# Performance work log

Hardware: AMD Instinct MI355X
Metric: run time of the kernel (lower is better)

Reference implementation:

```python
import jax, jax.numpy as jnp
import numpy as np

N_NODES = 100000
N_EDGES = 1600000
F_IN = 64
HIDDEN = 128
N_GRAPHS = 1024
EPS = 1e-5  # BatchNorm1d eps


def setup_inputs() -> dict:
    key = jax.random.key(0)
    ks = jax.random.split(key, 16)
    inp = {
        "x": jax.random.normal(ks[0], (N_NODES, F_IN), jnp.float32),
        "edge_index": jax.random.randint(ks[1], (2, N_EDGES), 0, N_NODES, dtype=jnp.int32),
        "edge_attr": jax.random.uniform(ks[2], (N_EDGES, 1), jnp.float32),
        "batch": jnp.sort(jax.random.randint(ks[3], (N_NODES,), 0, N_GRAPHS, dtype=jnp.int32)),
    }
    dims = [F_IN, HIDDEN, HIDDEN]
    for i in range(3):
        d_in = dims[i]
        kk = jax.random.split(ks[4 + i], 2)
        s = 1.0 / np.sqrt(d_in).astype(np.float32)
        inp[f"rel_w{i}"] = jax.random.uniform(kk[0], (d_in, HIDDEN), jnp.float32, -s, s)
        inp[f"rel_b{i}"] = jnp.zeros((HIDDEN,), jnp.float32)
        inp[f"root_w{i}"] = jax.random.uniform(kk[1], (d_in, HIDDEN), jnp.float32, -s, s)
        inp[f"bn_g{i}"] = jnp.ones((HIDDEN,), jnp.float32)
        inp[f"bn_b{i}"] = jnp.zeros((HIDDEN,), jnp.float32)
        inp[f"bn_m{i}"] = jnp.zeros((HIDDEN,), jnp.float32)
        inp[f"bn_v{i}"] = jnp.ones((HIDDEN,), jnp.float32)
    inp["head_w1"] = jax.random.uniform(ks[8], (HIDDEN, HIDDEN // 2), jnp.float32, -0.1, 0.1)
    inp["head_b1"] = jnp.zeros((HIDDEN // 2,), jnp.float32)
    inp["head_w2"] = jax.random.uniform(ks[9], (HIDDEN // 2, 1), jnp.float32, -0.1, 0.1)
    inp["head_b2"] = jnp.zeros((1,), jnp.float32)
    return inp


def _graph_conv(h, src, dst, ew, w_rel, b_rel, w_root):
    # PyG GraphConv (aggr='add'): lin_rel(sum_j e_ji * x_j) + lin_root(x_i)
    msg = h[src] * ew[:, None]                                   # [E, in] gather
    agg = jax.ops.segment_sum(msg, dst, num_segments=h.shape[0])  # [N, in] scatter-add
    return agg @ w_rel + b_rel + h @ w_root


def reference(x, edge_index, edge_attr, batch,
              rel_w0, rel_b0, root_w0, bn_g0, bn_b0, bn_m0, bn_v0,
              rel_w1, rel_b1, root_w1, bn_g1, bn_b1, bn_m1, bn_v1,
              rel_w2, rel_b2, root_w2, bn_g2, bn_b2, bn_m2, bn_v2,
              head_w1, head_b1, head_w2, head_b2):
    src, dst = edge_index[0], edge_index[1]
    ew = edge_attr[:, 0]
    layers = [
        (rel_w0, rel_b0, root_w0, bn_g0, bn_b0, bn_m0, bn_v0),
        (rel_w1, rel_b1, root_w1, bn_g1, bn_b1, bn_m1, bn_v1),
        (rel_w2, rel_b2, root_w2, bn_g2, bn_b2, bn_m2, bn_v2),
    ]
    h = x
    for (wr, br, wo, g, b, m, v) in layers:
        h = _graph_conv(h, src, dst, ew, wr, br, wo)
        # BatchNorm1d in eval mode (running stats) + ReLU; dropout is identity in eval
        h = jax.nn.relu((h - m) * (g * jax.lax.rsqrt(v + EPS)) + b)
    # global_mean_pool over graph assignment ids
    sums = jax.ops.segment_sum(h, batch, num_segments=N_GRAPHS)                       # [G, H]
    cnts = jax.ops.segment_sum(jnp.ones((h.shape[0],), h.dtype), batch, num_segments=N_GRAPHS)
    pooled = sums / jnp.maximum(cnts, 1.0)[:, None]
    hid = jax.nn.relu(pooled @ head_w1 + head_b1)
    out = hid @ head_w2 + head_b2
    return out[:, 0]
```

## Files before the change

kernel.cpp:

```cpp
#include <hip/hip_runtime.h>

#define N_NODES 100000
#define N_EDGES 1600000
#define F_IN 64
#define HIDDEN 128
#define N_GRAPHS 1024
#define EPS 1e-5f

typedef short short8 __attribute__((ext_vector_type(8)));
typedef float f32x4 __attribute__((ext_vector_type(4)));
typedef unsigned int uint;
typedef unsigned short ushort;

__device__ __forceinline__ ushort f2b(float f) {
    uint x = __float_as_uint(f);
    return (ushort)((x + 0x7fffu + ((x >> 16) & 1u)) >> 16);
}
__device__ __forceinline__ uint pack2(float a, float b) {
    return (uint)f2b(a) | ((uint)f2b(b) << 16);
}
__device__ __forceinline__ float b2f_lo(uint u) { return __uint_as_float(u << 16); }
__device__ __forceinline__ float b2f_hi(uint u) { return __uint_as_float(u & 0xffff0000u); }

#define NBLK_A 128
#define CHUNK ((N_EDGES + NBLK_A - 1) / NBLK_A)
#define BUCK_SHIFT 9
#define NBUCK ((N_NODES + 511) / 512)
#define SCAN_M (NBUCK * NBLK_A)


__global__ __launch_bounds__(256) void bin_count_kernel(const int* __restrict__ ei,
                                                        int* __restrict__ counts) {
    __shared__ int cnt[NBUCK];
    int blk = blockIdx.x, t = threadIdx.x;
    for (int i = t; i < NBUCK; i += 256) cnt[i] = 0;
    __syncthreads();
    int e0 = blk * CHUNK, e1 = min(e0 + CHUNK, N_EDGES);
    for (int e = e0 + t; e < e1; e += 256)
        atomicAdd(&cnt[ei[N_EDGES + e] >> BUCK_SHIFT], 1);
    __syncthreads();
    for (int i = t; i < NBUCK; i += 256) counts[i * NBLK_A + blk] = cnt[i];
}

__global__ __launch_bounds__(1024) void scan_counts_kernel(int* __restrict__ counts,
                                                           int* __restrict__ rowptr) {
    __shared__ int tot[1024];
    const int PT = (SCAN_M + 1023) / 1024;
    int t = threadIdx.x;
    int base = t * PT;
    int local[PT];
    int s = 0;
    #pragma unroll
    for (int i = 0; i < PT; ++i) {
        int idx = base + i;
        int v = (idx < SCAN_M) ? counts[idx] : 0;
        local[i] = s;
        s += v;
    }
    tot[t] = s;
    __syncthreads();
    int v = s;
    for (int off = 1; off < 1024; off <<= 1) {
        int x = (t >= off) ? tot[t - off] : 0;
        __syncthreads();
        tot[t] += x;
        __syncthreads();
    }
    int excl = tot[t] - v;
    #pragma unroll
    for (int i = 0; i < PT; ++i) {
        int idx = base + i;
        if (idx < SCAN_M) counts[idx] = excl + local[i];
    }
    if (t == 0) rowptr[N_NODES] = N_EDGES;
}

__global__ __launch_bounds__(256) void bin_scatter_kernel(const int* __restrict__ ei,
                                                          const float* __restrict__ ea,
                                                          const int* __restrict__ counts,
                                                          int* __restrict__ dstb,
                                                          int2* __restrict__ emb) {
    __shared__ int cur[NBUCK];
    int blk = blockIdx.x, t = threadIdx.x;
    for (int i = t; i < NBUCK; i += 256) cur[i] = counts[i * NBLK_A + blk];
    __syncthreads();
    int e0 = blk * CHUNK, e1 = min(e0 + CHUNK, N_EDGES);
    for (int e = e0 + t; e < e1; e += 256) {
        int s = ei[e], d = ei[N_EDGES + e];
        float w = ea[e];
        int p = atomicAdd(&cur[d >> BUCK_SHIFT], 1);
        dstb[p] = d;
        emb[p] = make_int2(s, __float_as_int(w));
    }
}

__global__ __launch_bounds__(1024) void bucket_build_kernel(const int* __restrict__ counts,
                                                            const int* __restrict__ dstb,
                                                            const int2* __restrict__ emb,
                                                            int* __restrict__ rowptr,
                                                            int2* __restrict__ em) {
    __shared__ int hist[512];
    __shared__ int cursor[512];
    int b = blockIdx.x, t = threadIdx.x;
    int beg = counts[b * NBLK_A];
    int end = (b + 1 < NBUCK) ? counts[(b + 1) * NBLK_A] : N_EDGES;
    int nbase = b << BUCK_SHIFT;
    int nnodes = min(512, N_NODES - nbase);

    if (t < 512) hist[t] = 0;
    __syncthreads();
    for (int e = beg + t; e < end; e += 1024)
        atomicAdd(&hist[dstb[e] & 511], 1);
    __syncthreads();

    int v = (t < 512) ? hist[t] : 0;
    for (int off = 1; off < 512; off <<= 1) {
        int x = (t < 512 && t >= off) ? hist[t - off] : 0;
        __syncthreads();
        if (t < 512) hist[t] += x;
        __syncthreads();
    }
    if (t < 512) {
        int excl = hist[t] - v;
        cursor[t] = beg + excl;
        if (t < nnodes) rowptr[nbase + t] = beg + excl;
    }
    __syncthreads();

    for (int e = beg + t; e < end; e += 1024) {
        int d = dstb[e];
        int2 m = emb[e];
        int p = atomicAdd(&cursor[d & 511], 1);
        em[p] = m;
    }
}


__global__ __launch_bounds__(256) void cvt_x_kernel(const float* __restrict__ x,
                                                    ushort* __restrict__ xb) {
    int i = blockIdx.x * 256 + threadIdx.x;
    if (i < N_NODES * 32) {
        float2 v = ((const float2*)x)[i];
        ((uint*)xb)[i] = pack2(v.x, v.y);
    }
}

__global__ __launch_bounds__(256) void cvt_w_kernel(const float* __restrict__ W0,
                                                    const float* __restrict__ W1,
                                                    int F, ushort* __restrict__ Wb) {
    int K = 2 * F;
    int idx = blockIdx.x * 256 + threadIdx.x;
    if (idx >= 64 * K) return;
    int c  = idx / (K / 2);
    int k2 = (idx % (K / 2)) * 2;
    float f0 = (k2 < F) ? W0[k2 * 128 + c] : W1[(k2 - F) * 128 + c];
    float f1 = (k2 + 1 < F) ? W0[(k2 + 1) * 128 + c] : W1[(k2 + 1 - F) * 128 + c];
    ((uint*)Wb)[idx] = pack2(f0, f1);
}


template <int F>
__global__ __launch_bounds__(256) void agg_kernel(const ushort* __restrict__ h,
                                                  const int* __restrict__ rowptr,
                                                  const int2* __restrict__ em,
                                                  ushort* __restrict__ agg) {
    int node = blockIdx.x * 4 + (threadIdx.x >> 6);
    int lane = threadIdx.x & 63;
    int g  = lane >> 4;
    int sl = lane & 15;
    int beg = rowptr[node], end = rowptr[node + 1];
    int e = beg;

    if (F == 128) {
        float acc[8] = {};
        for (; e + 8 <= end; e += 8) {
            int2 mA = em[e + g];
            int2 mB = em[e + 4 + g];
            uint4 vA = *(const uint4*)(h + (size_t)mA.x * 128 + sl * 8);
            uint4 vB = *(const uint4*)(h + (size_t)mB.x * 128 + sl * 8);
            float wA = __int_as_float(mA.y), wB = __int_as_float(mB.y);
            acc[0] = fmaf(b2f_lo(vA.x), wA, acc[0]);
            acc[1] = fmaf(b2f_hi(vA.x), wA, acc[1]);
            acc[2] = fmaf(b2f_lo(vA.y), wA, acc[2]);
            acc[3] = fmaf(b2f_hi(vA.y), wA, acc[3]);
            acc[4] = fmaf(b2f_lo(vA.z), wA, acc[4]);
            acc[5] = fmaf(b2f_hi(vA.z), wA, acc[5]);
            acc[6] = fmaf(b2f_lo(vA.w), wA, acc[6]);
            acc[7] = fmaf(b2f_hi(vA.w), wA, acc[7]);
            acc[0] = fmaf(b2f_lo(vB.x), wB, acc[0]);
            acc[1] = fmaf(b2f_hi(vB.x), wB, acc[1]);
            acc[2] = fmaf(b2f_lo(vB.y), wB, acc[2]);
            acc[3] = fmaf(b2f_hi(vB.y), wB, acc[3]);
            acc[4] = fmaf(b2f_lo(vB.z), wB, acc[4]);
            acc[5] = fmaf(b2f_hi(vB.z), wB, acc[5]);
            acc[6] = fmaf(b2f_lo(vB.w), wB, acc[6]);
            acc[7] = fmaf(b2f_hi(vB.w), wB, acc[7]);
        }
        for (; e < end; e += 4) {
            int ej = e + g;
            if (ej < end) {
                int2 m = em[ej];
                uint4 v = *(const uint4*)(h + (size_t)m.x * 128 + sl * 8);
                float w = __int_as_float(m.y);
                acc[0] = fmaf(b2f_lo(v.x), w, acc[0]);
                acc[1] = fmaf(b2f_hi(v.x), w, acc[1]);
                acc[2] = fmaf(b2f_lo(v.y), w, acc[2]);
                acc[3] = fmaf(b2f_hi(v.y), w, acc[3]);
                acc[4] = fmaf(b2f_lo(v.z), w, acc[4]);
                acc[5] = fmaf(b2f_hi(v.z), w, acc[5]);
                acc[6] = fmaf(b2f_lo(v.w), w, acc[6]);
                acc[7] = fmaf(b2f_hi(v.w), w, acc[7]);
            }
        }
        #pragma unroll
        for (int f = 0; f < 8; ++f) {
            acc[f] += __shfl_xor(acc[f], 16);
            acc[f] += __shfl_xor(acc[f], 32);
        }
        if (lane < 16) {
            uint4 o;
            o.x = pack2(acc[0], acc[1]);
            o.y = pack2(acc[2], acc[3]);
            o.z = pack2(acc[4], acc[5]);
            o.w = pack2(acc[6], acc[7]);
            *(uint4*)(agg + (size_t)node * 128 + sl * 8) = o;
        }
    } else {
        float acc[4] = {};
        for (; e + 8 <= end; e += 8) {
            int2 mA = em[e + g];
            int2 mB = em[e + 4 + g];
            uint2 vA = *(const uint2*)(h + (size_t)mA.x * 64 + sl * 4);
            uint2 vB = *(const uint2*)(h + (size_t)mB.x * 64 + sl * 4);
            float wA = __int_as_float(mA.y), wB = __int_as_float(mB.y);
            acc[0] = fmaf(b2f_lo(vA.x), wA, acc[0]);
            acc[1] = fmaf(b2f_hi(vA.x), wA, acc[1]);
            acc[2] = fmaf(b2f_lo(vA.y), wA, acc[2]);
            acc[3] = fmaf(b2f_hi(vA.y), wA, acc[3]);
            acc[0] = fmaf(b2f_lo(vB.x), wB, acc[0]);
            acc[1] = fmaf(b2f_hi(vB.x), wB, acc[1]);
            acc[2] = fmaf(b2f_lo(vB.y), wB, acc[2]);
            acc[3] = fmaf(b2f_hi(vB.y), wB, acc[3]);
        }
        for (; e < end; e += 4) {
            int ej = e + g;
            if (ej < end) {
                int2 m = em[ej];
                uint2 v = *(const uint2*)(h + (size_t)m.x * 64 + sl * 4);
                float w = __int_as_float(m.y);
                acc[0] = fmaf(b2f_lo(v.x), w, acc[0]);
                acc[1] = fmaf(b2f_hi(v.x), w, acc[1]);
                acc[2] = fmaf(b2f_lo(v.y), w, acc[2]);
                acc[3] = fmaf(b2f_hi(v.y), w, acc[3]);
            }
        }
        #pragma unroll
        for (int f = 0; f < 4; ++f) {
            acc[f] += __shfl_xor(acc[f], 16);
            acc[f] += __shfl_xor(acc[f], 32);
        }
        if (lane < 16) {
            uint2 o;
            o.x = pack2(acc[0], acc[1]);
            o.y = pack2(acc[2], acc[3]);
            *(uint2*)(agg + (size_t)node * 64 + sl * 4) = o;
        }
    }
}


template <int F>
__global__ __launch_bounds__(256, 2) void gemm_mfma(const ushort* __restrict__ A0,
                                                    const ushort* __restrict__ A1,
                                                    const ushort* __restrict__ Wb,
                                                    const float* __restrict__ bias,
                                                    const float* __restrict__ bng,
                                                    const float* __restrict__ bnb,
                                                    const float* __restrict__ bnm,
                                                    const float* __restrict__ bnv,
                                                    ushort* __restrict__ out) {
    constexpr int K = 2 * F;
    constexpr int LDW = K + 8;
    __shared__ ushort Wl[128 * LDW];

    int t = threadIdx.x;
    for (int idx = t; idx < 128 * (K / 8); idx += 256) {
        int c  = idx / (K / 8);
        int k8 = (idx % (K / 8)) * 8;
        *(short8*)&Wl[c * LDW + k8] = *(const short8*)&Wb[c * K + k8];
    }
    __syncthreads();

    int wave = t >> 6, lane = t & 63;
    int m = lane & 15, quad = lane >> 4;
    int r0 = blockIdx.x * 128 + wave * 32 + m;
    int r1 = r0 + 16;

    f32x4 acc0[8], acc1[8];
    #pragma unroll
    for (int i = 0; i < 8; ++i) { acc0[i] = (f32x4)(0.f); acc1[i] = (f32x4)(0.f); }

    auto loadA = [&](int row, int k0) -> short8 {
        short8 v = {};
        if (row < N_NODES)
            v = (k0 < F) ? *(const short8*)(A0 + (size_t)row * F + k0)
                         : *(const short8*)(A1 + (size_t)row * F + (k0 - F));
        return v;
    };

    short8 a0 = loadA(r0, quad * 8);
    short8 a1 = loadA(r1, quad * 8);
    for (int kc = 0; kc < K; kc += 32) {
        int k0 = kc + quad * 8;
        short8 na0 = {}, na1 = {};
        if (kc + 32 < K) {
            na0 = loadA(r0, k0 + 32);
            na1 = loadA(r1, k0 + 32);
        }
        #pragma unroll
        for (int ct = 0; ct < 8; ++ct) {
            short8 b = *(const short8*)&Wl[(ct * 16 + m) * LDW + k0];
            acc0[ct] = __builtin_amdgcn_mfma_f32_16x16x32_bf16(a0, b, acc0[ct], 0, 0, 0);
            acc1[ct] = __builtin_amdgcn_mfma_f32_16x16x32_bf16(a1, b, acc1[ct], 0, 0, 0);
        }
        a0 = na0; a1 = na1;
    }

    int rb0 = blockIdx.x * 128 + wave * 32 + quad * 4;
    #pragma unroll
    for (int ct = 0; ct < 8; ++ct) {
        int c = ct * 16 + m;
        float sc = bng[c] * rsqrtf(bnv[c] + EPS);
        float sh = bnb[c] - bnm[c] * sc;
        float bi = bias[c];
        #pragma unroll
        for (int reg = 0; reg < 4; ++reg) {
            int r = rb0 + reg;
            if (r < N_NODES) {
                float v = fmaxf(fmaf(acc0[ct][reg] + bi, sc, sh), 0.f);
                out[(size_t)r * 128 + c] = f2b(v);
            }
            int r2 = rb0 + 16 + reg;
            if (r2 < N_NODES) {
                float v = fmaxf(fmaf(acc1[ct][reg] + bi, sc, sh), 0.f);
                out[(size_t)r2 * 128 + c] = f2b(v);
            }
        }
    }
}


#define POOL_NODES 64
__global__ __launch_bounds__(256) void pool_kernel(const ushort* __restrict__ h,
                                                   const int* __restrict__ batch,
                                                   float* __restrict__ pooled) {
    __shared__ int gb[POOL_NODES];
    int b = blockIdx.x, t = threadIdx.x;
    int n0 = b * POOL_NODES;
    if (t < POOL_NODES) {
        int n = n0 + t;
        gb[t] = (n < N_NODES) ? batch[n] : -1;
    }
    __syncthreads();
    int f = t & 127;
    int half = t >> 7;
    float acc = 0.f;
    int gcur = -1;
    for (int i = half; i < POOL_NODES; i += 2) {
        int n = n0 + i;
        if (n >= N_NODES) break;
        int g = gb[i];
        if (g != gcur) {
            if (gcur >= 0) atomicAdd(&pooled[(size_t)gcur * 128 + f], acc);
            gcur = g;
            acc = 0.f;
        }
        acc += b2f_lo((uint)h[(size_t)n * 128 + f]);
    }
    if (gcur >= 0) atomicAdd(&pooled[(size_t)gcur * 128 + f], acc);
}


__global__ __launch_bounds__(64) void head_kernel(const float* __restrict__ pooled,
                                                  const int* __restrict__ batch,
                                                  const float* __restrict__ w1,
                                                  const float* __restrict__ b1,
                                                  const float* __restrict__ w2,
                                                  const float* __restrict__ b2,
                                                  float* __restrict__ out) {
    int g = blockIdx.x;
    int j = threadIdx.x;
    int lo = 0, hi = N_NODES;
    while (lo < hi) { int m = (lo + hi) >> 1; if (batch[m] <  g) lo = m + 1; else hi = m; }
    int start = lo;
    lo = 0; hi = N_NODES;
    while (lo < hi) { int m = (lo + hi) >> 1; if (batch[m] <= g) lo = m + 1; else hi = m; }
    float inv = 1.0f / fmaxf((float)(lo - start), 1.0f);

    float acc = b1[j];
    #pragma unroll 4
    for (int k = 0; k < 128; ++k)
        acc = fmaf(pooled[(size_t)g * 128 + k] * inv, w1[k * 64 + j], acc);
    float prod = fmaxf(acc, 0.f) * w2[j];
    #pragma unroll
    for (int off = 32; off > 0; off >>= 1)
        prod += __shfl_down(prod, off);
    if (j == 0) out[g] = prod + b2[0];
}


extern "C" void kernel_launch(void* const* d_in, const int* in_sizes, int n_in,
                              void* d_out, int out_size, void* d_ws, size_t ws_size,
                              hipStream_t stream) {
    const float* x     = (const float*)d_in[0];
    const int*   ei    = (const int*)d_in[1];
    const float* ea    = (const float*)d_in[2];
    const int*   batch = (const int*)d_in[3];
    const float* rel_w[3]  = {(const float*)d_in[4],  (const float*)d_in[11], (const float*)d_in[18]};
    const float* rel_b[3]  = {(const float*)d_in[5],  (const float*)d_in[12], (const float*)d_in[19]};
    const float* root_w[3] = {(const float*)d_in[6],  (const float*)d_in[13], (const float*)d_in[20]};
    const float* bn_g[3]   = {(const float*)d_in[7],  (const float*)d_in[14], (const float*)d_in[21]};
    const float* bn_b[3]   = {(const float*)d_in[8],  (const float*)d_in[15], (const float*)d_in[22]};
    const float* bn_m[3]   = {(const float*)d_in[9],  (const float*)d_in[16], (const float*)d_in[23]};
    const float* bn_v[3]   = {(const float*)d_in[10], (const float*)d_in[17], (const float*)d_in[24]};
    const float* head_w1 = (const float*)d_in[25];
    const float* head_b1 = (const float*)d_in[26];
    const float* head_w2 = (const float*)d_in[27];
    const float* head_b2 = (const float*)d_in[28];
    float* out = (float*)d_out;

    char* ws = (char*)d_ws;
    int*    rowptr = (int*)(ws + 0);
    int*    counts = (int*)(ws + 401408);
    int2*   em     = (int2*)(ws + 524288);
    ushort* xb     = (ushort*)(ws + 13631488);
    ushort* h_a    = (ushort*)(ws + 26431488);
    ushort* h_b    = (ushort*)(ws + 52031488);
    ushort* aggb   = (ushort*)(ws + 77631488);
    float*  pooled = (float*)(ws + 103231488);
    ushort* wb     = (ushort*)(ws + 103755776);
    int*    dstb = (int*)(ws + 77631488);
    int2*   emb  = (int2*)(ws + 84031488);

    ushort* wb0 = wb;
    ushort* wb1 = wb + 16384;
    ushort* wb2 = wb + 49152;

    hipMemsetAsync(pooled, 0, N_GRAPHS * HIDDEN * sizeof(float), stream);

    bin_count_kernel<<<NBLK_A, 256, 0, stream>>>(ei, counts);
    scan_counts_kernel<<<1, 1024, 0, stream>>>(counts, rowptr);
    bin_scatter_kernel<<<NBLK_A, 256, 0, stream>>>(ei, ea, counts, dstb, emb);
    bucket_build_kernel<<<NBUCK, 1024, 0, stream>>>(counts, dstb, emb, rowptr, em);
    cvt_x_kernel<<<(N_NODES * 32 + 255) / 256, 256, 0, stream>>>(x, xb);
    cvt_w_kernel<<<(64 * 128 + 255) / 256, 256, 0, stream>>>(rel_w[0], root_w[0], 64,  wb0);
    cvt_w_kernel<<<(64 * 256 + 255) / 256, 256, 0, stream>>>(rel_w[1], root_w[1], 128, wb1);
    cvt_w_kernel<<<(64 * 256 + 255) / 256, 256, 0, stream>>>(rel_w[2], root_w[2], 128, wb2);

    const int AGG_BLOCKS  = N_NODES / 4;
    const int GEMM_BLOCKS = (N_NODES + 127) / 128;

    agg_kernel<64><<<AGG_BLOCKS, 256, 0, stream>>>(xb, rowptr, em, aggb);
    gemm_mfma<64><<<GEMM_BLOCKS, 256, 0, stream>>>(aggb, xb, wb0, rel_b[0],
                                                   bn_g[0], bn_b[0], bn_m[0], bn_v[0], h_a);
    agg_kernel<128><<<AGG_BLOCKS, 256, 0, stream>>>(h_a, rowptr, em, aggb);
    gemm_mfma<128><<<GEMM_BLOCKS, 256, 0, stream>>>(aggb, h_a, wb1, rel_b[1],
                                                    bn_g[1], bn_b[1], bn_m[1], bn_v[1], h_b);
    agg_kernel<128><<<AGG_BLOCKS, 256, 0, stream>>>(h_b, rowptr, em, aggb);
    gemm_mfma<128><<<GEMM_BLOCKS, 256, 0, stream>>>(aggb, h_b, wb2, rel_b[2],
                                                    bn_g[2], bn_b[2], bn_m[2], bn_v[2], h_a);

    pool_kernel<<<(N_NODES + POOL_NODES - 1) / POOL_NODES, 256, 0, stream>>>(h_a, batch, pooled);
    head_kernel<<<N_GRAPHS, 64, 0, stream>>>(pooled, batch, head_w1, head_b1, head_w2, head_b2, out);
}
```

Before: 527.6 us.

## Fuse prep kernels, split scan across blocks, pack edge data, widen pool loads

Merges the x/weight bf16 conversions and the pooled zeroing into one prep kernel, which removes several launches and a memset. The single-block count scan becomes a three-kernel reduce/scan/apply across multiple blocks. Edge binning now packs a bf16 weight and the low destination bits into one word, dropping the separate dstb array and its traffic, at the cost of rounding edge weights to bf16 earlier. The pool kernel reads two features per thread with 32-bit loads.

```diff
diff --git a/kernel.cpp b/kernel.cpp
--- a/kernel.cpp
+++ b/kernel.cpp
@@ -27,6 +27,7 @@
 #define BUCK_SHIFT 9
 #define NBUCK ((N_NODES + 511) / 512)
 #define SCAN_M (NBUCK * NBLK_A)
+#define SCAN_T ((SCAN_M + 1023) / 1024)
 
 
 __global__ __launch_bounds__(256) void bin_count_kernel(const int* __restrict__ ei,
@@ -42,43 +43,53 @@
     for (int i = t; i < NBUCK; i += 256) counts[i * NBLK_A + blk] = cnt[i];
 }
 
-__global__ __launch_bounds__(1024) void scan_counts_kernel(int* __restrict__ counts,
-                                                           int* __restrict__ rowptr) {
-    __shared__ int tot[1024];
-    const int PT = (SCAN_M + 1023) / 1024;
-    int t = threadIdx.x;
-    int base = t * PT;
-    int local[PT];
-    int s = 0;
+__global__ __launch_bounds__(1024) void sc_reduce_kernel(const int* __restrict__ counts,
+                                                         int* __restrict__ partial) {
+    __shared__ int lds[16];
+    int b = blockIdx.x, t = threadIdx.x;
+    int i = b * 1024 + t;
+    int v = (i < SCAN_M) ? counts[i] : 0;
     #pragma unroll
-    for (int i = 0; i < PT; ++i) {
-        int idx = base + i;
-        int v = (idx < SCAN_M) ? counts[idx] : 0;
-        local[i] = s;
-        s += v;
-    }
-    tot[t] = s;
-    __syncthreads();
-    int v = s;
+    for (int off = 32; off > 0; off >>= 1) v += __shfl_down(v, off);
+    if ((t & 63) == 0) lds[t >> 6] = v;
+    __syncthreads();
+    if (t == 0) {
+        int s = 0;
+        #pragma unroll
+        for (int j = 0; j < 16; ++j) s += lds[j];
+        partial[b] = s;
+    }
+}
+
+__global__ __launch_bounds__(64) void sc_small_kernel(int* __restrict__ partial,
+                                                      int* __restrict__ rowptr) {
+    if (threadIdx.x == 0) {
+        int s = 0;
+        for (int j = 0; j < SCAN_T; ++j) { int v = partial[j]; partial[j] = s; s += v; }
+        rowptr[N_NODES] = N_EDGES;
+    }
+}
+
+__global__ __launch_bounds__(1024) void sc_apply_kernel(int* __restrict__ counts,
+                                                        const int* __restrict__ partial) {
+    __shared__ int lds[1024];
+    int b = blockIdx.x, t = threadIdx.x;
+    int i = b * 1024 + t;
+    int v = (i < SCAN_M) ? counts[i] : 0;
+    lds[t] = v;
+    __syncthreads();
     for (int off = 1; off < 1024; off <<= 1) {
-        int x = (t >= off) ? tot[t - off] : 0;
+        int x = (t >= off) ? lds[t - off] : 0;
         __syncthreads();
-        tot[t] += x;
+        lds[t] += x;
         __syncthreads();
     }
-    int excl = tot[t] - v;
-    #pragma unroll
-    for (int i = 0; i < PT; ++i) {
-        int idx = base + i;
-        if (idx < SCAN_M) counts[idx] = excl + local[i];
-    }
-    if (t == 0) rowptr[N_NODES] = N_EDGES;
+    if (i < SCAN_M) counts[i] = lds[t] - v + partial[b];
 }
 
 __global__ __launch_bounds__(256) void bin_scatter_kernel(const int* __restrict__ ei,
                                                           const float* __restrict__ ea,
                                                           const int* __restrict__ counts,
-                                                          int* __restrict__ dstb,
                                                           int2* __restrict__ emb) {
     __shared__ int cur[NBUCK];
     int blk = blockIdx.x, t = threadIdx.x;
@@ -87,15 +98,13 @@
     int e0 = blk * CHUNK, e1 = min(e0 + CHUNK, N_EDGES);
     for (int e = e0 + t; e < e1; e += 256) {
         int s = ei[e], d = ei[N_EDGES + e];
-        float w = ea[e];
+        uint y = ((uint)f2b(ea[e]) << 16) | (uint)(d & 511);
         int p = atomicAdd(&cur[d >> BUCK_SHIFT], 1);
-        dstb[p] = d;
-        emb[p] = make_int2(s, __float_as_int(w));
+        emb[p] = make_int2(s, (int)y);
     }
 }
 
 __global__ __launch_bounds__(1024) void bucket_build_kernel(const int* __restrict__ counts,
-                                                            const int* __restrict__ dstb,
                                                             const int2* __restrict__ emb,
                                                             int* __restrict__ rowptr,
                                                             int2* __restrict__ em) {
@@ -110,7 +119,7 @@
     if (t < 512) hist[t] = 0;
     __syncthreads();
     for (int e = beg + t; e < end; e += 1024)
-        atomicAdd(&hist[dstb[e] & 511], 1);
+        atomicAdd(&hist[(uint)emb[e].y & 511u], 1);
     __syncthreads();
 
     int v = (t < 512) ? hist[t] : 0;
@@ -128,34 +137,50 @@
     __syncthreads();
 
     for (int e = beg + t; e < end; e += 1024) {
-        int d = dstb[e];
         int2 m = emb[e];
-        int p = atomicAdd(&cursor[d & 511], 1);
-        em[p] = m;
-    }
-}
-
-
-__global__ __launch_bounds__(256) void cvt_x_kernel(const float* __restrict__ x,
-                                                    ushort* __restrict__ xb) {
-    int i = blockIdx.x * 256 + threadIdx.x;
-    if (i < N_NODES * 32) {
-        float2 v = ((const float2*)x)[i];
-        ((uint*)xb)[i] = pack2(v.x, v.y);
-    }
-}
-
-__global__ __launch_bounds__(256) void cvt_w_kernel(const float* __restrict__ W0,
-                                                    const float* __restrict__ W1,
-                                                    int F, ushort* __restrict__ Wb) {
+        int p = atomicAdd(&cursor[(uint)m.y & 511u], 1);
+        em[p] = make_int2(m.x, (int)((uint)m.y & 0xffff0000u));
+    }
+}
+
+
+#define PREP_X   (N_NODES * 32)
+#define PREP_W0  8192
+#define PREP_W1  16384
+#define PREP_W2  16384
+#define PREP_PZ  (N_GRAPHS * HIDDEN)
+#define PREP_TOT (PREP_X + PREP_W0 + PREP_W1 + PREP_W2 + PREP_PZ)
+
+__device__ __forceinline__ void cvt_w_elem(const float* W0, const float* W1, int F,
+                                           int idx, uint* out) {
     int K = 2 * F;
-    int idx = blockIdx.x * 256 + threadIdx.x;
-    if (idx >= 64 * K) return;
     int c  = idx / (K / 2);
     int k2 = (idx % (K / 2)) * 2;
     float f0 = (k2 < F) ? W0[k2 * 128 + c] : W1[(k2 - F) * 128 + c];
     float f1 = (k2 + 1 < F) ? W0[(k2 + 1) * 128 + c] : W1[(k2 + 1 - F) * 128 + c];
-    ((uint*)Wb)[idx] = pack2(f0, f1);
+    out[idx] = pack2(f0, f1);
+}
+
+__global__ __launch_bounds__(256) void prep_kernel(const float* __restrict__ x, uint* __restrict__ xb,
+                                                   const float* __restrict__ rw0, const float* __restrict__ ow0,
+                                                   const float* __restrict__ rw1, const float* __restrict__ ow1,
+                                                   const float* __restrict__ rw2, const float* __restrict__ ow2,
+                                                   uint* __restrict__ wb0, uint* __restrict__ wb1,
+                                                   uint* __restrict__ wb2, float* __restrict__ pooled) {
+    int i = blockIdx.x * 256 + threadIdx.x;
+    if (i < PREP_X) {
+        float2 v = ((const float2*)x)[i];
+        xb[i] = pack2(v.x, v.y);
+        return;
+    }
+    i -= PREP_X;
+    if (i < PREP_W0) { cvt_w_elem(rw0, ow0, 64, i, wb0); return; }
+    i -= PREP_W0;
+    if (i < PREP_W1) { cvt_w_elem(rw1, ow1, 128, i, wb1); return; }
+    i -= PREP_W1;
+    if (i < PREP_W2) { cvt_w_elem(rw2, ow2, 128, i, wb2); return; }
+    i -= PREP_W2;
+    if (i < PREP_PZ) pooled[i] = 0.f;
 }
 
 
@@ -362,22 +387,31 @@
         gb[t] = (n < N_NODES) ? batch[n] : -1;
     }
     __syncthreads();
-    int f = t & 127;
-    int half = t >> 7;
-    float acc = 0.f;
+    int f2 = t & 63;
+    int q  = t >> 6;
+    const uint* hp = (const uint*)h;
+    float alo = 0.f, ahi = 0.f;
     int gcur = -1;
-    for (int i = half; i < POOL_NODES; i += 2) {
+    for (int i = q; i < POOL_NODES; i += 4) {
         int n = n0 + i;
         if (n >= N_NODES) break;
         int g = gb[i];
         if (g != gcur) {
-            if (gcur >= 0) atomicAdd(&pooled[(size_t)gcur * 128 + f], acc);
+            if (gcur >= 0) {
+                atomicAdd(&pooled[(size_t)gcur * 128 + f2 * 2], alo);
+                atomicAdd(&pooled[(size_t)gcur * 128 + f2 * 2 + 1], ahi);
+            }
             gcur = g;
-            acc = 0.f;
-        }
-        acc += b2f_lo((uint)h[(size_t)n * 128 + f]);
-    }
-    if (gcur >= 0) atomicAdd(&pooled[(size_t)gcur * 128 + f], acc);
+            alo = 0.f; ahi = 0.f;
+        }
+        uint u = hp[(size_t)n * 64 + f2];
+        alo += b2f_lo(u);
+        ahi += b2f_hi(u);
+    }
+    if (gcur >= 0) {
+        atomicAdd(&pooled[(size_t)gcur * 128 + f2 * 2], alo);
+        atomicAdd(&pooled[(size_t)gcur * 128 + f2 * 2 + 1], ahi);
+    }
 }
 
 
@@ -430,32 +464,32 @@
     float* out = (float*)d_out;
 
     char* ws = (char*)d_ws;
-    int*    rowptr = (int*)(ws + 0);
-    int*    counts = (int*)(ws + 401408);
-    int2*   em     = (int2*)(ws + 524288);
-    ushort* xb     = (ushort*)(ws + 13631488);
-    ushort* h_a    = (ushort*)(ws + 26431488);
-    ushort* h_b    = (ushort*)(ws + 52031488);
-    ushort* aggb   = (ushort*)(ws + 77631488);
-    float*  pooled = (float*)(ws + 103231488);
-    ushort* wb     = (ushort*)(ws + 103755776);
-    int*    dstb = (int*)(ws + 77631488);
-    int2*   emb  = (int2*)(ws + 84031488);
+    int*    rowptr  = (int*)(ws + 0);
+    int*    counts  = (int*)(ws + 401408);
+    int*    partial = (int*)(ws + 503808);
+    int2*   em      = (int2*)(ws + 524288);
+    ushort* xb      = (ushort*)(ws + 13631488);
+    ushort* h_a     = (ushort*)(ws + 26431488);
+    ushort* h_b     = (ushort*)(ws + 52031488);
+    ushort* aggb    = (ushort*)(ws + 77631488);
+    float*  pooled  = (float*)(ws + 103231488);
+    ushort* wb      = (ushort*)(ws + 103755776);
+    int2*   emb = (int2*)(ws + 77631488);
 
     ushort* wb0 = wb;
     ushort* wb1 = wb + 16384;
     ushort* wb2 = wb + 49152;
 
-    hipMemsetAsync(pooled, 0, N_GRAPHS * HIDDEN * sizeof(float), stream);
+    prep_kernel<<<(PREP_TOT + 255) / 256, 256, 0, stream>>>(
+        x, (uint*)xb, rel_w[0], root_w[0], rel_w[1], root_w[1], rel_w[2], root_w[2],
+        (uint*)wb0, (uint*)wb1, (uint*)wb2, pooled);
 
     bin_count_kernel<<<NBLK_A, 256, 0, stream>>>(ei, counts);
-    scan_counts_kernel<<<1, 1024, 0, stream>>>(counts, rowptr);
-    bin_scatter_kernel<<<NBLK_A, 256, 0, stream>>>(ei, ea, counts, dstb, emb);
-    bucket_build_kernel<<<NBUCK, 1024, 0, stream>>>(counts, dstb, emb, rowptr, em);
-    cvt_x_kernel<<<(N_NODES * 32 + 255) / 256, 256, 0, stream>>>(x, xb);
-    cvt_w_kernel<<<(64 * 128 + 255) / 256, 256, 0, stream>>>(rel_w[0], root_w[0], 64,  wb0);
-    cvt_w_kernel<<<(64 * 256 + 255) / 256, 256, 0, stream>>>(rel_w[1], root_w[1], 128, wb1);
-    cvt_w_kernel<<<(64 * 256 + 255) / 256, 256, 0, stream>>>(rel_w[2], root_w[2], 128, wb2);
+    sc_reduce_kernel<<<SCAN_T, 1024, 0, stream>>>(counts, partial);
+    sc_small_kernel<<<1, 64, 0, stream>>>(partial, rowptr);
+    sc_apply_kernel<<<SCAN_T, 1024, 0, stream>>>(counts, partial);
+    bin_scatter_kernel<<<NBLK_A, 256, 0, stream>>>(ei, ea, counts, emb);
+    bucket_build_kernel<<<NBUCK, 1024, 0, stream>>>(counts, emb, rowptr, em);
 
     const int AGG_BLOCKS  = N_NODES / 4;
     const int GEMM_BLOCKS = (N_NODES + 127) / 128;
```

After: 490.1 us. 1.08x faster.
